# Performance work log

Measured on AMD Instinct MI355X. Metric: run time of the kernel, lower is better.

Reference implementation:

```python
import jax, jax.numpy as jnp
import numpy as np

ENT_TYPES = 9
INNER_DIM = 64
BIG_NEG = 1e12


def _rope_tables(seq_len, dim, dtype):
    # sinusoidal_position_embedding: interleaved [sin, cos] of pos * 10000^(-2i/d)
    pos = jnp.arange(seq_len, dtype=jnp.float32)[:, None]            # [S,1]
    inv_freq = jnp.power(10000.0, -2.0 * jnp.arange(dim // 2, dtype=jnp.float32) / dim)
    ang = pos * inv_freq                                             # [S,D/2]
    emb = jnp.stack([jnp.sin(ang), jnp.cos(ang)], axis=-1).reshape(seq_len, dim)  # [S,D]
    cos_pos = jnp.repeat(emb[:, 1::2], 2, axis=-1).astype(dtype)     # [S,D]
    sin_pos = jnp.repeat(emb[:, ::2], 2, axis=-1).astype(dtype)      # [S,D]
    return cos_pos, sin_pos


def _rotate_half(x):
    # stack([-x[...,1::2], x[...,::2]], -1).reshape(x.shape)
    return jnp.stack([-x[..., 1::2], x[..., ::2]], axis=-1).reshape(x.shape)


def setup_inputs() -> dict:
    key = jax.random.key(0)
    k1, k2 = jax.random.split(key)
    B, S, H = 16, 512, 1024
    last_hidden_state = jax.random.normal(k1, (B, S, H), dtype=jnp.float32)
    padding_mask = jnp.ones((B, S), dtype=jnp.float32)
    W = jax.random.normal(k2, (H, ENT_TYPES * INNER_DIM * 2), dtype=jnp.float32) * (1.0 / np.sqrt(H))
    b = jnp.zeros((ENT_TYPES * INNER_DIM * 2,), dtype=jnp.float32)
    return {"last_hidden_state": last_hidden_state, "padding_mask": padding_mask, "W": W, "b": b}


def reference(last_hidden_state, padding_mask, W, b):
    B, S, _ = last_hidden_state.shape
    H, D = ENT_TYPES, INNER_DIM
    out = last_hidden_state @ W + b                 # [B,S,H*2D]
    out = out.reshape(B, S, H, 2 * D)
    qw, kw = out[..., :D], out[..., D:]             # [B,S,H,D]

    cos_pos, sin_pos = _rope_tables(S, D, qw.dtype)  # [S,D]
    cos_pos = cos_pos[None, :, None, :]
    sin_pos = sin_pos[None, :, None, :]
    qw = qw * cos_pos + _rotate_half(qw) * sin_pos
    kw = kw * cos_pos + _rotate_half(kw) * sin_pos

    logits = jnp.einsum('bmhd,bnhd->bhmn', qw, kw)   # [B,H,S,S]
    pad = padding_mask[:, None, None, :]             # mask over key dim
    logits = logits * pad - (1.0 - pad) * BIG_NEG
    tril = jnp.tril(jnp.ones((S, S), dtype=logits.dtype), -1)
    logits = logits - tril * BIG_NEG
    return logits / jnp.sqrt(jnp.asarray(D, dtype=logits.dtype))
```

## Files before the change

### kernel.cpp

```cpp
#include <hip/hip_runtime.h>

#define EN 9
#define DD 64
#define SS 512
#define HH 1024
#define NOUT 1152

typedef float f32x4 __attribute__((ext_vector_type(4)));
typedef short short8v __attribute__((ext_vector_type(8)));

#define GPTR(p) ((const __attribute__((address_space(1))) void*)(p))
#define LPTR(p) ((__attribute__((address_space(3))) void*)(p))

__device__ inline unsigned short f2bf(float f) {
  unsigned int u = __float_as_uint(f);
  return (unsigned short)((u + 0x7FFFu + ((u >> 16) & 1u)) >> 16);
}

__device__ inline int pk4_fp8(float a, float b, float c, float d) {
  int v = __builtin_amdgcn_cvt_pk_fp8_f32(a, b, 0, false);
  v = __builtin_amdgcn_cvt_pk_fp8_f32(c, d, v, true);
  return v;
}

__global__ __launch_bounds__(256) void prep_kernel(
    const float* __restrict__ W, const float* __restrict__ X,
    unsigned char* __restrict__ Wf8, unsigned char* __restrict__ Xf8,
    float* __restrict__ ctab, float* __restrict__ stab) {
  if (blockIdx.x < 288u) {
    __shared__ float t[64][65];
    const int k0 = (blockIdx.x / 18) * 64;
    const int n0 = (blockIdx.x % 18) * 64;
    const int r = threadIdx.x >> 6;
    const int c = threadIdx.x & 63;
#pragma unroll
    for (int i = 0; i < 16; ++i) {
      const int kk = (i << 2) + r;
      t[kk][c] = W[(size_t)(k0 + kk) * NOUT + n0 + c];
    }
    __syncthreads();
#pragma unroll
    for (int i = 0; i < 2; ++i) {
      const int p = (i << 8) + threadIdx.x;
      const int n = p >> 3, cc = p & 7;
      const int kk = cc << 3;
      const int lo = pk4_fp8(t[kk][n], t[kk + 1][n], t[kk + 2][n], t[kk + 3][n]);
      const int hi =
          pk4_fp8(t[kk + 4][n], t[kk + 5][n], t[kk + 6][n], t[kk + 7][n]);
      const int gn = n0 + n;
      int2 v;
      v.x = lo;
      v.y = hi;
      *(int2*)(Wf8 + (size_t)gn * HH + k0 + ((cc ^ (gn & 7)) << 3)) = v;
    }
  } else if (blockIdx.x < 304u) {
    const int bt = blockIdx.x - 288;
#pragma unroll
    for (int j = 0; j < 4; ++j) {
      const int id = bt * 1024 + j * 256 + threadIdx.x;
      const int s = id >> 5, i = id & 31;
      const float freq = expf(-(float)(2 * i) * (9.210340371976184f / 64.0f));
      const float ang = (float)s * freq;
      ctab[id] = cosf(ang);
      stab[id] = sinf(ang);
    }
  } else {
    const int bt = blockIdx.x - 304;
#pragma unroll
    for (int j = 0; j < 4; ++j) {
      const int C = bt * 1024 + (j << 8) + threadIdx.x;
      const int row = C >> 7, c = C & 127;
      const float4 v0 = *(const float4*)(X + (size_t)C * 8);
      const float4 v1 = *(const float4*)(X + (size_t)C * 8 + 4);
      int2 v;
      v.x = pk4_fp8(v0.x, v0.y, v0.z, v0.w);
      v.y = pk4_fp8(v1.x, v1.y, v1.z, v1.w);
      *(int2*)(Xf8 + (size_t)row * HH + ((c >> 3) << 6) +
               (((c ^ row) & 7) << 3)) = v;
    }
  }
}

__global__ __launch_bounds__(256, 3) void proj_rope_kernel(
    const unsigned char* __restrict__ Xf8, const unsigned char* __restrict__ Wf8,
    const float* __restrict__ bias, const float* __restrict__ ctab,
    const float* __restrict__ stab, unsigned short* __restrict__ QK) {
  __shared__ __align__(16) unsigned char sm[49152];
  const int tid = threadIdx.x;
  const int lane = tid & 63;
  const int wid = tid >> 6;
  const int wr = wid >> 1, wc = wid & 1;
  const int f = blockIdx.x;
  const int wkr = (f & 7) * 72 + (f >> 3);
  const int m0 = (wkr / 9) << 7;
  const int n0 = (wkr % 9) << 7;

  f32x4 acc[4][4];
#pragma unroll
  for (int i = 0; i < 4; ++i)
#pragma unroll
    for (int j = 0; j < 4; ++j) acc[i][j] = (f32x4){0.f, 0.f, 0.f, 0.f};

#define STAGE(BUF, KT)                                                       \
  {                                                                          \
    const int kt_ = (KT);                                                    \
    unsigned char* dst_ = sm + (BUF)*16384;                                  \
    _Pragma("unroll") for (int it = 0; it < 2; ++it) {                       \
      const int u_ = (it << 8) + tid;                                        \
      const int r_ = u_ >> 2, g_ = u_ & 3;                                   \
      __builtin_amdgcn_global_load_lds(                                      \
          GPTR(Xf8 + (size_t)(m0 + r_) * HH + kt_ + (g_ << 4)),              \
          LPTR(dst_ + (((it << 8) + (wid << 6)) << 4)), 16, 0, 0);           \
      __builtin_amdgcn_global_load_lds(                                      \
          GPTR(Wf8 + (size_t)(n0 + r_) * HH + kt_ + (g_ << 4)),              \
          LPTR(dst_ + 8192 + (((it << 8) + (wid << 6)) << 4)), 16, 0, 0);    \
    }                                                                        \
  }

#define COMPUTE(BUF)                                                         \
  {                                                                          \
    const unsigned char* smc_ = sm + (BUF)*16384;                            \
    __builtin_amdgcn_s_setprio(1);                                           \
    _Pragma("unroll") for (int kb = 0; kb < 2; ++kb) {                       \
      long aL[4], bL[4];                                                     \
      const int c8 = (kb << 2) + (lane >> 4);                                \
      _Pragma("unroll") for (int i = 0; i < 4; ++i) {                        \
        const int ra = (wr << 6) + (i << 4) + (lane & 15);                   \
        aL[i] = *(const long*)(smc_ + (ra << 6) + (((c8 ^ ra) & 7) << 3));   \
        const int rb = (wc << 6) + (i << 4) + (lane & 15);                   \
        bL[i] = *(const long*)(smc_ + 8192 + (rb << 6) +                     \
                               (((c8 ^ rb) & 7) << 3));                      \
      }                                                                      \
      _Pragma("unroll") for (int mi = 0; mi < 4; ++mi)                       \
          _Pragma("unroll") for (int ni = 0; ni < 4; ++ni) acc[mi][ni] =     \
          __builtin_amdgcn_mfma_f32_16x16x32_fp8_fp8(aL[mi], bL[ni],         \
                                                     acc[mi][ni], 0, 0, 0);  \
    }                                                                        \
    __builtin_amdgcn_s_setprio(0);                                           \
  }

  STAGE(0, 0)
  STAGE(1, 64)
#pragma unroll 1
  for (int t = 0; t < 14; ++t) {
    STAGE((t + 2) % 3, (t + 2) << 6)
    asm volatile("s_waitcnt vmcnt(8)" ::: "memory");
    __builtin_amdgcn_s_barrier();
    __builtin_amdgcn_sched_barrier(0);
    COMPUTE(t % 3)
    __builtin_amdgcn_sched_barrier(0);
    __builtin_amdgcn_s_barrier();
  }
  asm volatile("s_waitcnt vmcnt(4)" ::: "memory");
  __builtin_amdgcn_s_barrier();
  __builtin_amdgcn_sched_barrier(0);
  COMPUTE(2)
  __builtin_amdgcn_sched_barrier(0);
  __builtin_amdgcn_s_barrier();
  asm volatile("s_waitcnt vmcnt(0)" ::: "memory");
  __builtin_amdgcn_s_barrier();
  __builtin_amdgcn_sched_barrier(0);
  COMPUTE(0)

  __syncthreads();
  float* scr = (float*)sm;
  const int erow = tid >> 3;
  const int ec8 = (tid & 7) << 1;
#pragma unroll
  for (int mi = 0; mi < 4; ++mi) {
#pragma unroll
    for (int ni = 0; ni < 4; ++ni) {
      const int col = (wc << 6) + (ni << 4) + (lane & 15);
#pragma unroll
      for (int r = 0; r < 4; ++r) {
        const int row = (wr << 4) + ((lane >> 4) << 2) + r;
        scr[row * 132 + col] = acc[mi][ni][r];
      }
    }
    __syncthreads();
    const int m = m0 + ((erow >> 4) << 6) + (mi << 4) + (erow & 15);
    const int s = m & (SS - 1);
    const int bb = m >> 9;
#pragma unroll
    for (int sl = 0; sl < 2; ++sl) {
      const int c8 = ec8 + sl;
      const int ncol = c8 << 3;
      const int n = n0 + ncol;
      const int h = n >> 7;
      const int t = (n >> 6) & 1;
      const int d0 = n & 63;
      const float4 va = *(const float4*)&scr[erow * 132 + ncol];
      const float4 vb = *(const float4*)&scr[erow * 132 + ncol + 4];
      const float4 bia = *(const float4*)&bias[n];
      const float4 bib = *(const float4*)&bias[n + 4];
      const float4 cs = *(const float4*)&ctab[(s << 5) + (d0 >> 1)];
      const float4 sn = *(const float4*)&stab[(s << 5) + (d0 >> 1)];
      const float e0 = va.x + bia.x, o0 = va.y + bia.y;
      const float e1 = va.z + bia.z, o1 = va.w + bia.w;
      const float e2 = vb.x + bib.x, o2 = vb.y + bib.y;
      const float e3 = vb.z + bib.z, o3 = vb.w + bib.w;
      short8v ov;
      ov[0] = (short)f2bf(e0 * cs.x - o0 * sn.x);
      ov[1] = (short)f2bf(o0 * cs.x + e0 * sn.x);
      ov[2] = (short)f2bf(e1 * cs.y - o1 * sn.y);
      ov[3] = (short)f2bf(o1 * cs.y + e1 * sn.y);
      ov[4] = (short)f2bf(e2 * cs.z - o2 * sn.z);
      ov[5] = (short)f2bf(o2 * cs.z + e2 * sn.z);
      ov[6] = (short)f2bf(e3 * cs.w - o3 * sn.w);
      ov[7] = (short)f2bf(o3 * cs.w + e3 * sn.w);
      *(short8v*)&QK[(((size_t)(bb * EN + h) * 2 + t) * SS + s) * DD + d0] = ov;
    }
    __syncthreads();
  }
}

__global__ __launch_bounds__(256, 4) void logits_kernel(
    const unsigned short* __restrict__ QK, const float* __restrict__ pmask,
    float* __restrict__ out) {
  __shared__ __align__(16) unsigned char sm[32768];
  const int tid = threadIdx.x;
  const int lane = tid & 63;
  const int wid = tid >> 6;
  const int wr = wid >> 1, wc = wid & 1;
  const int f = blockIdx.x;
  const int wkr = (f & 7) * 288 + (f >> 3);
  const int bh = wkr >> 4;
  const int bb = bh / EN;
  const int tm = (wkr >> 2) & 3, tn = wkr & 3;
  const int mq0 = tm << 7, nk0 = tn << 7;
  const unsigned short* Qb = QK + (size_t)bh * 2 * SS * DD;
  const unsigned short* Kb = Qb + SS * DD;

#pragma unroll
  for (int it = 0; it < 4; ++it) {
    const int q = it * 256 + tid;
    const int r = q >> 3, cl = q & 7;
    const int cs = cl ^ (r & 7);
    __builtin_amdgcn_global_load_lds(
        GPTR(Qb + (size_t)(mq0 + r) * DD + (cs << 3)),
        LPTR(sm + ((it * 256 + wid * 64) << 4)), 16, 0, 0);
    __builtin_amdgcn_global_load_lds(
        GPTR(Kb + (size_t)(nk0 + r) * DD + (cs << 3)),
        LPTR(sm + 16384 + ((it * 256 + wid * 64) << 4)), 16, 0, 0);
  }
  __syncthreads();

  f32x4 acc[4][4];
#pragma unroll
  for (int i = 0; i < 4; ++i)
#pragma unroll
    for (int j = 0; j < 4; ++j) acc[i][j] = (f32x4){0.f, 0.f, 0.f, 0.f};

  typedef short bf16x8 __attribute__((ext_vector_type(8)));
#pragma unroll
  for (int kb = 0; kb < 2; ++kb) {
    bf16x8 af[4], bfr[4];
    const int ca = (kb << 2) + (lane >> 4);
#pragma unroll
    for (int i = 0; i < 4; ++i) {
      const int ra = (wr << 6) + (i << 4) + (lane & 15);
      af[i] = *(const bf16x8*)(sm + (ra << 7) + ((ca ^ (ra & 7)) << 4));
      const int rb = (wc << 6) + (i << 4) + (lane & 15);
      bfr[i] =
          *(const bf16x8*)(sm + 16384 + (rb << 7) + ((ca ^ (rb & 7)) << 4));
    }
#pragma unroll
    for (int mi = 0; mi < 4; ++mi)
#pragma unroll
      for (int ni = 0; ni < 4; ++ni)
        acc[mi][ni] = __builtin_amdgcn_mfma_f32_16x16x32_bf16(
            af[mi], bfr[ni], acc[mi][ni], 0, 0, 0);
  }

#pragma unroll
  for (int mi = 0; mi < 4; ++mi) {
#pragma unroll
    for (int ni = 0; ni < 4; ++ni) {
      const int n = nk0 + (wc << 6) + (ni << 4) + (lane & 15);
      const float pd = pmask[bb * SS + n];
      const float sub = (1.0f - pd) * 1e12f;
#pragma unroll
      for (int r = 0; r < 4; ++r) {
        const int m = mq0 + (wr << 6) + (mi << 4) + ((lane >> 4) << 2) + r;
        float v = acc[mi][ni][r] * pd - sub;
        if (m > n) v -= 1e12f;
        out[((size_t)bh * SS + m) * SS + n] = v * 0.125f;
      }
    }
  }
}

extern "C" void kernel_launch(void* const* d_in, const int* in_sizes, int n_in,
                              void* d_out, int out_size, void* d_ws,
                              size_t ws_size, hipStream_t stream) {
  const float* X = (const float*)d_in[0];
  const float* pm = (const float*)d_in[1];
  const float* W = (const float*)d_in[2];
  const float* bias = (const float*)d_in[3];
  float* out = (float*)d_out;
  unsigned char* ws = (unsigned char*)d_ws;
  unsigned short* QK = (unsigned short*)ws;
  unsigned char* Wf8 = ws + 18874368;
  float* ctab = (float*)(ws + 20054016);
  float* stab = (float*)(ws + 20119552);
  unsigned char* Xf8 = ws + 20185088;

  prep_kernel<<<dim3(1328), dim3(256), 0, stream>>>(W, X, Wf8, Xf8, ctab, stab);
  proj_rope_kernel<<<dim3(576), dim3(256), 0, stream>>>(Xf8, Wf8, bias, ctab,
                                                        stab, QK);
  logits_kernel<<<dim3(2304), dim3(256), 0, stream>>>(QK, pm, out);
}
```

Measured before the change: 63.19 us.

## Store Q/K in fp8 and use fp8 MFMA for logits, double-buffer projection

The projection kernel now writes rotated Q and K as swizzled fp8 instead of bf16. Q is pre-scaled by 1/8, so the logits epilogue drops its final multiply and the mask constants are rescaled to match. The logits kernel loads half as many bytes into LDS and uses the fp8 16x16x32 MFMA. The projection pipeline goes from triple to double buffering with less LDS, raising the occupancy target from 3 to 4 blocks. This cuts QK workspace traffic and LDS footprint but lowers the precision of the logits, and the output write, which dominates traffic, is unchanged.

```diff
diff --git a/kernel.cpp b/kernel.cpp
--- a/kernel.cpp
+++ b/kernel.cpp
@@ -7,20 +7,19 @@
 #define NOUT 1152
 
 typedef float f32x4 __attribute__((ext_vector_type(4)));
-typedef short short8v __attribute__((ext_vector_type(8)));
 
 #define GPTR(p) ((const __attribute__((address_space(1))) void*)(p))
 #define LPTR(p) ((__attribute__((address_space(3))) void*)(p))
-
-__device__ inline unsigned short f2bf(float f) {
-  unsigned int u = __float_as_uint(f);
-  return (unsigned short)((u + 0x7FFFu + ((u >> 16) & 1u)) >> 16);
-}
 
 __device__ inline int pk4_fp8(float a, float b, float c, float d) {
   int v = __builtin_amdgcn_cvt_pk_fp8_f32(a, b, 0, false);
   v = __builtin_amdgcn_cvt_pk_fp8_f32(c, d, v, true);
   return v;
+}
+
+__device__ inline unsigned short f2bf(float f) {
+  unsigned int u = __float_as_uint(f);
+  return (unsigned short)((u + 0x7FFFu + ((u >> 16) & 1u)) >> 16);
 }
 
 __global__ __launch_bounds__(256) void prep_kernel(
@@ -81,11 +80,11 @@
   }
 }
 
-__global__ __launch_bounds__(256, 3) void proj_rope_kernel(
+__global__ __launch_bounds__(256, 4) void proj_rope_kernel(
     const unsigned char* __restrict__ Xf8, const unsigned char* __restrict__ Wf8,
     const float* __restrict__ bias, const float* __restrict__ ctab,
-    const float* __restrict__ stab, unsigned short* __restrict__ QK) {
-  __shared__ __align__(16) unsigned char sm[49152];
+    const float* __restrict__ stab, unsigned char* __restrict__ QK) {
+  __shared__ __align__(16) unsigned char sm[32768];
   const int tid = threadIdx.x;
   const int lane = tid & 63;
   const int wid = tid >> 6;
@@ -140,27 +139,20 @@
   }
 
   STAGE(0, 0)
-  STAGE(1, 64)
 #pragma unroll 1
-  for (int t = 0; t < 14; ++t) {
-    STAGE((t + 2) % 3, (t + 2) << 6)
-    asm volatile("s_waitcnt vmcnt(8)" ::: "memory");
+  for (int t = 0; t < 15; ++t) {
+    STAGE((t + 1) & 1, (t + 1) << 6)
+    asm volatile("s_waitcnt vmcnt(4)" ::: "memory");
     __builtin_amdgcn_s_barrier();
     __builtin_amdgcn_sched_barrier(0);
-    COMPUTE(t % 3)
+    COMPUTE(t & 1)
     __builtin_amdgcn_sched_barrier(0);
     __builtin_amdgcn_s_barrier();
   }
-  asm volatile("s_waitcnt vmcnt(4)" ::: "memory");
-  __builtin_amdgcn_s_barrier();
-  __builtin_amdgcn_sched_barrier(0);
-  COMPUTE(2)
-  __builtin_amdgcn_sched_barrier(0);
-  __builtin_amdgcn_s_barrier();
   asm volatile("s_waitcnt vmcnt(0)" ::: "memory");
   __builtin_amdgcn_s_barrier();
   __builtin_amdgcn_sched_barrier(0);
-  COMPUTE(0)
+  COMPUTE(1)
 
   __syncthreads();
   float* scr = (float*)sm;
@@ -189,6 +181,7 @@
       const int h = n >> 7;
       const int t = (n >> 6) & 1;
       const int d0 = n & 63;
+      const float scale = (t == 0) ? 0.125f : 1.0f;
       const float4 va = *(const float4*)&scr[erow * 132 + ncol];
       const float4 vb = *(const float4*)&scr[erow * 132 + ncol + 4];
       const float4 bia = *(const float4*)&bias[n];
@@ -199,25 +192,27 @@
       const float e1 = va.z + bia.z, o1 = va.w + bia.w;
       const float e2 = vb.x + bib.x, o2 = vb.y + bib.y;
       const float e3 = vb.z + bib.z, o3 = vb.w + bib.w;
-      short8v ov;
-      ov[0] = (short)f2bf(e0 * cs.x - o0 * sn.x);
-      ov[1] = (short)f2bf(o0 * cs.x + e0 * sn.x);
-      ov[2] = (short)f2bf(e1 * cs.y - o1 * sn.y);
-      ov[3] = (short)f2bf(o1 * cs.y + e1 * sn.y);
-      ov[4] = (short)f2bf(e2 * cs.z - o2 * sn.z);
-      ov[5] = (short)f2bf(o2 * cs.z + e2 * sn.z);
-      ov[6] = (short)f2bf(e3 * cs.w - o3 * sn.w);
-      ov[7] = (short)f2bf(o3 * cs.w + e3 * sn.w);
-      *(short8v*)&QK[(((size_t)(bb * EN + h) * 2 + t) * SS + s) * DD + d0] = ov;
+      int2 ov;
+      ov.x = pk4_fp8((e0 * cs.x - o0 * sn.x) * scale,
+                     (o0 * cs.x + e0 * sn.x) * scale,
+                     (e1 * cs.y - o1 * sn.y) * scale,
+                     (o1 * cs.y + e1 * sn.y) * scale);
+      ov.y = pk4_fp8((e2 * cs.z - o2 * sn.z) * scale,
+                     (o2 * cs.z + e2 * sn.z) * scale,
+                     (e3 * cs.w - o3 * sn.w) * scale,
+                     (o3 * cs.w + e3 * sn.w) * scale);
+      const int cswz = (((d0 >> 3) ^ (s & 7)) << 3);
+      *(int2*)(QK + (((size_t)(bb * EN + h) * 2 + t) * SS + s) * DD + cswz) =
+          ov;
     }
     __syncthreads();
   }
 }
 
 __global__ __launch_bounds__(256, 4) void logits_kernel(
-    const unsigned short* __restrict__ QK, const float* __restrict__ pmask,
+    const unsigned char* __restrict__ QK, const float* __restrict__ pmask,
     float* __restrict__ out) {
-  __shared__ __align__(16) unsigned char sm[32768];
+  __shared__ __align__(16) unsigned char sm[16384];
   const int tid = threadIdx.x;
   const int lane = tid & 63;
   const int wid = tid >> 6;
@@ -228,20 +223,19 @@
   const int bb = bh / EN;
   const int tm = (wkr >> 2) & 3, tn = wkr & 3;
   const int mq0 = tm << 7, nk0 = tn << 7;
-  const unsigned short* Qb = QK + (size_t)bh * 2 * SS * DD;
-  const unsigned short* Kb = Qb + SS * DD;
-
-#pragma unroll
-  for (int it = 0; it < 4; ++it) {
-    const int q = it * 256 + tid;
-    const int r = q >> 3, cl = q & 7;
-    const int cs = cl ^ (r & 7);
+  const unsigned char* Qb = QK + (size_t)bh * 2 * SS * DD;
+  const unsigned char* Kb = Qb + SS * DD;
+
+#pragma unroll
+  for (int it = 0; it < 2; ++it) {
+    const int u = (it << 8) + tid;
+    const int r = u >> 2, g = u & 3;
     __builtin_amdgcn_global_load_lds(
-        GPTR(Qb + (size_t)(mq0 + r) * DD + (cs << 3)),
-        LPTR(sm + ((it * 256 + wid * 64) << 4)), 16, 0, 0);
+        GPTR(Qb + (size_t)(mq0 + r) * DD + (g << 4)),
+        LPTR(sm + (((it << 8) + (wid << 6)) << 4)), 16, 0, 0);
     __builtin_amdgcn_global_load_lds(
-        GPTR(Kb + (size_t)(nk0 + r) * DD + (cs << 3)),
-        LPTR(sm + 16384 + ((it * 256 + wid * 64) << 4)), 16, 0, 0);
+        GPTR(Kb + (size_t)(nk0 + r) * DD + (g << 4)),
+        LPTR(sm + 8192 + (((it << 8) + (wid << 6)) << 4)), 16, 0, 0);
   }
   __syncthreads();
 
@@ -251,25 +245,23 @@
 #pragma unroll
     for (int j = 0; j < 4; ++j) acc[i][j] = (f32x4){0.f, 0.f, 0.f, 0.f};
 
-  typedef short bf16x8 __attribute__((ext_vector_type(8)));
 #pragma unroll
   for (int kb = 0; kb < 2; ++kb) {
-    bf16x8 af[4], bfr[4];
-    const int ca = (kb << 2) + (lane >> 4);
+    long aL[4], bL[4];
+    const int c8 = (kb << 2) + (lane >> 4);
 #pragma unroll
     for (int i = 0; i < 4; ++i) {
       const int ra = (wr << 6) + (i << 4) + (lane & 15);
-      af[i] = *(const bf16x8*)(sm + (ra << 7) + ((ca ^ (ra & 7)) << 4));
+      aL[i] = *(const long*)(sm + (ra << 6) + (((c8 ^ ra) & 7) << 3));
       const int rb = (wc << 6) + (i << 4) + (lane & 15);
-      bfr[i] =
-          *(const bf16x8*)(sm + 16384 + (rb << 7) + ((ca ^ (rb & 7)) << 4));
+      bL[i] = *(const long*)(sm + 8192 + (rb << 6) + (((c8 ^ rb) & 7) << 3));
     }
 #pragma unroll
     for (int mi = 0; mi < 4; ++mi)
 #pragma unroll
       for (int ni = 0; ni < 4; ++ni)
-        acc[mi][ni] = __builtin_amdgcn_mfma_f32_16x16x32_bf16(
-            af[mi], bfr[ni], acc[mi][ni], 0, 0, 0);
+        acc[mi][ni] = __builtin_amdgcn_mfma_f32_16x16x32_fp8_fp8(
+            aL[mi], bL[ni], acc[mi][ni], 0, 0, 0);
   }
 
 #pragma unroll
@@ -278,13 +270,13 @@
     for (int ni = 0; ni < 4; ++ni) {
       const int n = nk0 + (wc << 6) + (ni << 4) + (lane & 15);
       const float pd = pmask[bb * SS + n];
-      const float sub = (1.0f - pd) * 1e12f;
+      const float sub = (1.0f - pd) * 1.25e11f;
 #pragma unroll
       for (int r = 0; r < 4; ++r) {
         const int m = mq0 + (wr << 6) + (mi << 4) + ((lane >> 4) << 2) + r;
         float v = acc[mi][ni][r] * pd - sub;
-        if (m > n) v -= 1e12f;
-        out[((size_t)bh * SS + m) * SS + n] = v * 0.125f;
+        if (m > n) v -= 1.25e11f;
+        out[((size_t)bh * SS + m) * SS + n] = v;
       }
     }
   }
@@ -299,11 +291,11 @@
   const float* bias = (const float*)d_in[3];
   float* out = (float*)d_out;
   unsigned char* ws = (unsigned char*)d_ws;
-  unsigned short* QK = (unsigned short*)ws;
-  unsigned char* Wf8 = ws + 18874368;
-  float* ctab = (float*)(ws + 20054016);
-  float* stab = (float*)(ws + 20119552);
-  unsigned char* Xf8 = ws + 20185088;
+  unsigned char* QK = ws;
+  unsigned char* Wf8 = ws + 9437184;
+  float* ctab = (float*)(ws + 10616832);
+  float* stab = (float*)(ws + 10682368);
+  unsigned char* Xf8 = ws + 10747904;
 
   prep_kernel<<<dim3(1328), dim3(256), 0, stream>>>(W, X, Wf8, Xf8, ctab, stab);
   proj_rope_kernel<<<dim3(576), dim3(256), 0, stream>>>(Xf8, Wf8, bias, ctab,
```

Result: no change. 62.72 us (-0.7%).
